# Optimization experiments

Measured on AMD Instinct MI355X. Metric: run time of the kernel, lower is better.

The kernel has to match this reference:

```python
import jax, jax.numpy as jnp
import numpy as np

N, E, D, H, C = 50000, 1600000, 256, 8, 32

def setup_inputs() -> dict:
    key = jax.random.key(0)
    ks = jax.random.split(key, 7)
    feat = jax.random.normal(ks[0], (N, D), dtype=jnp.float32)
    edge_weight = jax.random.uniform(ks[1], (E,), dtype=jnp.float32)
    W_lin = jax.random.normal(ks[2], (D, H * C), dtype=jnp.float32) * (1.0 / np.sqrt(D))
    att_l = jax.random.normal(ks[3], (1, H, C), dtype=jnp.float32) * (1.0 / np.sqrt(H))
    att_r = jax.random.normal(ks[4], (1, H, C), dtype=jnp.float32) * (1.0 / np.sqrt(H))
    W_res = jax.random.normal(ks[5], (D, H * C), dtype=jnp.float32) * (1.0 / np.sqrt(D))
    edge_index = jax.random.randint(ks[6], (2, E), 0, N, dtype=jnp.int32)
    return {"feat": feat, "edge_weight": edge_weight, "W_lin": W_lin,
            "att_l": att_l, "att_r": att_r, "W_res": W_res, "edge_index": edge_index}

def reference(feat, edge_weight, W_lin, att_l, att_r, W_res, edge_index):
    n_nodes = feat.shape[0]
    h, c = att_l.shape[1], att_l.shape[2]
    src, dst = edge_index[0], edge_index[1]
    # node projection: [N, H, C]
    x = (feat @ W_lin).reshape(n_nodes, h, c)
    alpha_l = (x * att_l).sum(-1)  # [N, H]
    alpha_r = (x * att_r).sum(-1)  # [N, H]
    # per-edge scores [E, H]
    alpha = alpha_l[src] + alpha_r[dst]
    alpha = edge_weight[:, None] * alpha
    alpha = jnp.where(alpha > 0, alpha, 0.2 * alpha)  # leaky_relu(0.2)
    # segment softmax over destination nodes
    amax = jax.lax.stop_gradient(jax.ops.segment_max(alpha, dst, num_segments=n_nodes))
    ex = jnp.exp(alpha - amax[dst])
    denom = jax.ops.segment_sum(ex, dst, num_segments=n_nodes)
    coeff = ex / (denom[dst] + 1e-16)  # [E, H]
    # weighted message aggregation
    msg = x[src] * coeff[:, :, None]  # [E, H, C]
    agg = jax.ops.segment_sum(msg, dst, num_segments=n_nodes)  # [N, H, C]
    out = jax.nn.elu(agg).reshape(n_nodes, h * c)
    out = out + feat @ W_res  # residual
    return out
```

## Files before the change

### kernel.cpp

```cpp
#include <hip/hip_runtime.h>
#include <stdint.h>

#define D_DIM 256
#define NPAD  640

typedef __bf16 bf16x8 __attribute__((ext_vector_type(8)));
typedef float  f32x4  __attribute__((ext_vector_type(4)));

__device__ __forceinline__ float bf2f(unsigned short u) {
  union { unsigned int i; float f; } cv; cv.i = ((unsigned int)u) << 16; return cv.f;
}
__device__ __forceinline__ unsigned short f2bf(float f) {
  union { float f; unsigned int i; } cv; cv.f = f;
  unsigned int i = cv.i;
  unsigned int lsb = (i >> 16) & 1u;
  i += 0x7fffu + lsb;
  return (unsigned short)(i >> 16);
}
__device__ __forceinline__ void gld16(const void* gptr, void* lptr) {
  __builtin_amdgcn_global_load_lds(
      (const __attribute__((address_space(1))) unsigned int*)gptr,
      (__attribute__((address_space(3))) unsigned int*)lptr, 16, 0, 0);
}

__global__ __launch_bounds__(256) void cvt_feat(const float* __restrict__ f,
                                                unsigned short* __restrict__ o, int n) {
  int i = (blockIdx.x * 256 + threadIdx.x) * 8;
  if (i >= n) return;
  float4 v0 = *(const float4*)(f + i);
  float4 v1 = *(const float4*)(f + i + 4);
  ushort4 a, b;
  a.x = f2bf(v0.x); a.y = f2bf(v0.y); a.z = f2bf(v0.z); a.w = f2bf(v0.w);
  b.x = f2bf(v1.x); b.y = f2bf(v1.y); b.z = f2bf(v1.z); b.w = f2bf(v1.w);
  *(ushort4*)(o + i) = a;
  *(ushort4*)(o + i + 4) = b;
}

__global__ __launch_bounds__(256) void prep_bt(
    const float* __restrict__ W_lin, const float* __restrict__ W_res,
    const float* __restrict__ att_l, const float* __restrict__ att_r,
    unsigned short* __restrict__ Bt) {
  int idx = blockIdx.x * 256 + threadIdx.x;
  if (idx >= NPAD * D_DIM) return;
  int n = idx >> 8, k = idx & 255;
  float v = 0.f;
  if (n < 256) v = W_lin[k * 256 + n];
  else if (n < 512) v = W_res[k * 256 + (n - 256)];
  else if (n < 520) {
    int h = n - 512; float s = 0.f;
    #pragma unroll
    for (int c = 0; c < 32; ++c) s += W_lin[k * 256 + h * 32 + c] * att_l[h * 32 + c];
    v = s;
  } else if (n < 528) {
    int h = n - 520; float s = 0.f;
    #pragma unroll
    for (int c = 0; c < 32; ++c) s += W_lin[k * 256 + h * 32 + c] * att_r[h * 32 + c];
    v = s;
  }
  Bt[idx] = f2bf(v);
}

__global__ __launch_bounds__(256) void gemm_mfma(
    const unsigned short* __restrict__ A,
    const unsigned short* __restrict__ Bt,
    float* __restrict__ out, unsigned short* __restrict__ xbf,
    float* __restrict__ alpha_l, float* __restrict__ alpha_r, int M) {
  __shared__ unsigned short As[128 * 32];
  __shared__ unsigned short Bs[128 * 32];
  int tid  = threadIdx.x;
  int w    = tid >> 6, lane = tid & 63;
  int bm   = blockIdx.x * 128, bn = blockIdx.y * 128;
  int wm   = (w & 1) * 64, wn = (w >> 1) * 64;
  int l16  = lane & 15, quad = lane >> 4;

  f32x4 acc[4][4] = {};

  int srow = w * 32 + (lane >> 2);
  int koff = (lane & 3) * 8;

  for (int k0 = 0; k0 < 256; k0 += 32) {
    #pragma unroll
    for (int i = 0; i < 2; ++i) {
      int r  = srow + i * 16;
      int rg = bm + r; if (rg > M - 1) rg = M - 1;
      gld16(A  + (size_t)rg * 256 + k0 + koff, &As[(w * 32 + i * 16) * 32]);
      gld16(Bt + (size_t)(bn + r) * 256 + k0 + koff, &Bs[(w * 32 + i * 16) * 32]);
    }
    __syncthreads();
    bf16x8 a[4], b[4];
    #pragma unroll
    for (int mi = 0; mi < 4; ++mi)
      a[mi] = *(const bf16x8*)&As[(wm + mi * 16 + l16) * 32 + quad * 8];
    #pragma unroll
    for (int ni = 0; ni < 4; ++ni)
      b[ni] = *(const bf16x8*)&Bs[(wn + ni * 16 + l16) * 32 + quad * 8];
    #pragma unroll
    for (int mi = 0; mi < 4; ++mi)
      #pragma unroll
      for (int ni = 0; ni < 4; ++ni)
        acc[mi][ni] = __builtin_amdgcn_mfma_f32_16x16x32_bf16(a[mi], b[ni], acc[mi][ni], 0, 0, 0);
    __syncthreads();
  }

  #pragma unroll
  for (int mi = 0; mi < 4; ++mi) {
    #pragma unroll
    for (int r = 0; r < 4; ++r) {
      int row = bm + wm + mi * 16 + quad * 4 + r;
      if (row >= M) continue;
      #pragma unroll
      for (int ni = 0; ni < 4; ++ni) {
        int n = bn + wn + ni * 16 + l16;
        float v = acc[mi][ni][r];
        if (n < 256)      xbf[(size_t)row * 256 + n] = f2bf(v);
        else if (n < 512) out[(size_t)row * 256 + (n - 256)] = v;
        else if (n < 520) alpha_l[row * 8 + (n - 512)] = v;
        else if (n < 528) alpha_r[row * 8 + (n - 520)] = v;
      }
    }
  }
}

__global__ __launch_bounds__(256) void hist_kernel(const int* __restrict__ dst,
                                                   int* __restrict__ cnt,
                                                   int* __restrict__ rank, int E) {
  int e = blockIdx.x * 256 + threadIdx.x;
  if (e < E) rank[e] = atomicAdd(&cnt[dst[e]], 1);
}

__global__ __launch_bounds__(256) void scan_partial(const int* __restrict__ cnt,
                                                    int* __restrict__ bsum, int N) {
  __shared__ int s[256];
  int t = threadIdx.x;
  int i = blockIdx.x * 256 + t;
  s[t] = (i < N) ? cnt[i] : 0;
  __syncthreads();
  for (int off = 128; off > 0; off >>= 1) {
    if (t < off) s[t] += s[t + off];
    __syncthreads();
  }
  if (t == 0) bsum[blockIdx.x] = s[0];
}

__global__ __launch_bounds__(256) void scan_top(int* __restrict__ bsum, int nb) {
  __shared__ int s[256];
  int t = threadIdx.x;
  int v = (t < nb) ? bsum[t] : 0;
  s[t] = v;
  __syncthreads();
  for (int off = 1; off < 256; off <<= 1) {
    int u = (t >= off) ? s[t - off] : 0;
    __syncthreads();
    s[t] += u;
    __syncthreads();
  }
  if (t < nb) bsum[t] = s[t] - v;
}

__global__ __launch_bounds__(256) void scan_apply(const int* __restrict__ cnt,
                                                  const int* __restrict__ bsum,
                                                  int* __restrict__ row_ptr, int N) {
  __shared__ int s[256];
  int t = threadIdx.x;
  int i = blockIdx.x * 256 + t;
  int v = (i < N) ? cnt[i] : 0;
  s[t] = v;
  __syncthreads();
  for (int off = 1; off < 256; off <<= 1) {
    int u = (t >= off) ? s[t - off] : 0;
    __syncthreads();
    s[t] += u;
    __syncthreads();
  }
  int excl = bsum[blockIdx.x] + s[t] - v;
  if (i < N) {
    row_ptr[i] = excl;
    if (i == N - 1) row_ptr[N] = excl + v;
  }
}

__global__ __launch_bounds__(256) void scatter_kernel(
    const int* __restrict__ eidx, const float* __restrict__ ew,
    const int* __restrict__ row_ptr, const int* __restrict__ rank,
    int2* __restrict__ pairs, int E) {
  int e = blockIdx.x * 256 + threadIdx.x;
  if (e < E) {
    int d = eidx[E + e];
    int pos = row_ptr[d] + rank[e];
    int2 p; p.x = eidx[e]; p.y = __float_as_int(ew[e]);
    pairs[pos] = p;
  }
}

__global__ __launch_bounds__(256) void agg_kernel(
    const int* __restrict__ row_ptr, const int2* __restrict__ pairs,
    const float* __restrict__ alpha_l, const float* __restrict__ alpha_r,
    const unsigned short* __restrict__ xbf, float* __restrict__ out, int N) {
  int node = blockIdx.x * 4 + (threadIdx.x >> 6);
  if (node >= N) return;
  int lane = threadIdx.x & 63;
  int h  = lane >> 3;
  int cb = lane << 2;

  int beg = row_ptr[node], end = row_ptr[node + 1];
  float arv = alpha_r[node * 8 + h];
  float l = 0.f;
  float ac0 = 0.f, ac1 = 0.f, ac2 = 0.f, ac3 = 0.f;
  int last = end - 1;

  for (int jg = beg; jg < end; jg += 4) {
    int idx[4];
    #pragma unroll
    for (int u = 0; u < 4; ++u) {
      int t = jg + u; idx[u] = (t < last) ? t : last;
    }
    int2 q[4];
    #pragma unroll
    for (int u = 0; u < 4; ++u) q[u] = pairs[idx[u]];
    float al[4];
    #pragma unroll
    for (int u = 0; u < 4; ++u) al[u] = alpha_l[(size_t)q[u].x * 8 + h];
    ushort4 xv[4];
    #pragma unroll
    for (int u = 0; u < 4; ++u)
      xv[u] = *(const ushort4*)(xbf + ((size_t)q[u].x << 8) + cb);
    #pragma unroll
    for (int u = 0; u < 4; ++u) {
      float a = __int_as_float(q[u].y) * (al[u] + arv);
      a = (a > 0.f) ? a : 0.2f * a;
      float p = __expf(a);
      p = (jg + u < end) ? p : 0.f;
      l += p;
      ac0 = fmaf(p, bf2f(xv[u].x), ac0);
      ac1 = fmaf(p, bf2f(xv[u].y), ac1);
      ac2 = fmaf(p, bf2f(xv[u].z), ac2);
      ac3 = fmaf(p, bf2f(xv[u].w), ac3);
    }
  }
  float r = 1.0f / (l + 1e-16f);
  float o0 = ac0 * r, o1 = ac1 * r, o2 = ac2 * r, o3 = ac3 * r;
  o0 = (o0 > 0.f) ? o0 : expm1f(o0);
  o1 = (o1 > 0.f) ? o1 : expm1f(o1);
  o2 = (o2 > 0.f) ? o2 : expm1f(o2);
  o3 = (o3 > 0.f) ? o3 : expm1f(o3);
  float4* op = (float4*)(out + ((size_t)node << 8) + cb);
  float4 res = *op;
  res.x += o0; res.y += o1; res.z += o2; res.w += o3;
  *op = res;
}

extern "C" void kernel_launch(void* const* d_in, const int* in_sizes, int n_in,
                              void* d_out, int out_size, void* d_ws, size_t ws_size,
                              hipStream_t stream) {
  const float* feat  = (const float*)d_in[0];
  const float* ew    = (const float*)d_in[1];
  const float* W_lin = (const float*)d_in[2];
  const float* att_l = (const float*)d_in[3];
  const float* att_r = (const float*)d_in[4];
  const float* W_res = (const float*)d_in[5];
  const int*   eidx  = (const int*)d_in[6];
  float* out = (float*)d_out;

  int N = in_sizes[0] / D_DIM;
  int E = in_sizes[1];

  char* p = (char*)d_ws;
  auto alloc = [&](size_t bytes) {
    char* r = p; p += (bytes + 255) & ~(size_t)255; return r;
  };
  unsigned short* xbf  = (unsigned short*)alloc((size_t)N * 256 * 2);
  unsigned short* fb   = (unsigned short*)alloc((size_t)N * 256 * 2);
  float* alpha_l       = (float*)alloc((size_t)N * 8 * 4);
  float* alpha_r       = (float*)alloc((size_t)N * 8 * 4);
  unsigned short* Bt   = (unsigned short*)alloc((size_t)NPAD * D_DIM * 2);
  int*   row_ptr       = (int*)alloc((size_t)(N + 1) * 4);
  int*   cnt           = (int*)alloc((size_t)N * 4);
  int*   rank          = (int*)alloc((size_t)E * 4);
  int*   bsum          = (int*)alloc(1024);
  int2*  pairs         = (int2*)fb;

  int nb = (N + 255) / 256;

  hipMemsetAsync(cnt, 0, (size_t)N * 4, stream);

  cvt_feat<<<(N * 256 / 8 + 255) / 256, 256, 0, stream>>>(feat, fb, N * 256);
  prep_bt<<<(NPAD * D_DIM + 255) / 256, 256, 0, stream>>>(W_lin, W_res, att_l, att_r, Bt);

  hist_kernel<<<(E + 255) / 256, 256, 0, stream>>>(eidx + E, cnt, rank, E);
  scan_partial<<<nb, 256, 0, stream>>>(cnt, bsum, N);
  scan_top<<<1, 256, 0, stream>>>(bsum, nb);
  scan_apply<<<nb, 256, 0, stream>>>(cnt, bsum, row_ptr, N);

  dim3 ggrid((N + 127) / 128, NPAD / 128);
  gemm_mfma<<<ggrid, 256, 0, stream>>>(fb, Bt, out, xbf, alpha_l, alpha_r, N);

  scatter_kernel<<<(E + 255) / 256, 256, 0, stream>>>(eidx, ew, row_ptr, rank, pairs, E);

  agg_kernel<<<(N + 3) / 4, 256, 0, stream>>>(row_ptr, pairs, alpha_l, alpha_r, xbf, out, N);
}
```

Measured before the change: 425.5 us.

## Fuse setup kernels, co-launch GEMM with edge scatter, unroll aggregation by 8

Merges feature conversion, weight packing and the destination histogram into one launch using block-index ranges. The GEMM and the edge scatter share one launch, with pairs moved to their own workspace buffer so the scatter no longer overwrites the bf16 features the GEMM reads. Aggregation now unrolls 8 edges per iteration for more gathers in flight and skips nodes with no edges. Intent is fewer launches and overlap of independent work; the cost is a larger workspace, a fallback path when it does not fit, and higher register pressure in aggregation.

Result: no change. 419.5 us (-1.4%).

```diff
diff --git a/kernel.cpp b/kernel.cpp
--- a/kernel.cpp
+++ b/kernel.cpp
@@ -23,109 +23,46 @@
       (__attribute__((address_space(3))) unsigned int*)lptr, 16, 0, 0);
 }
 
-__global__ __launch_bounds__(256) void cvt_feat(const float* __restrict__ f,
-                                                unsigned short* __restrict__ o, int n) {
-  int i = (blockIdx.x * 256 + threadIdx.x) * 8;
-  if (i >= n) return;
-  float4 v0 = *(const float4*)(f + i);
-  float4 v1 = *(const float4*)(f + i + 4);
-  ushort4 a, b;
-  a.x = f2bf(v0.x); a.y = f2bf(v0.y); a.z = f2bf(v0.z); a.w = f2bf(v0.w);
-  b.x = f2bf(v1.x); b.y = f2bf(v1.y); b.z = f2bf(v1.z); b.w = f2bf(v1.w);
-  *(ushort4*)(o + i) = a;
-  *(ushort4*)(o + i + 4) = b;
-}
-
-__global__ __launch_bounds__(256) void prep_bt(
+__global__ __launch_bounds__(256) void setup_fused(
+    const float* __restrict__ feat, unsigned short* __restrict__ fb,
     const float* __restrict__ W_lin, const float* __restrict__ W_res,
     const float* __restrict__ att_l, const float* __restrict__ att_r,
-    unsigned short* __restrict__ Bt) {
-  int idx = blockIdx.x * 256 + threadIdx.x;
-  if (idx >= NPAD * D_DIM) return;
-  int n = idx >> 8, k = idx & 255;
-  float v = 0.f;
-  if (n < 256) v = W_lin[k * 256 + n];
-  else if (n < 512) v = W_res[k * 256 + (n - 256)];
-  else if (n < 520) {
-    int h = n - 512; float s = 0.f;
-    #pragma unroll
-    for (int c = 0; c < 32; ++c) s += W_lin[k * 256 + h * 32 + c] * att_l[h * 32 + c];
-    v = s;
-  } else if (n < 528) {
-    int h = n - 520; float s = 0.f;
-    #pragma unroll
-    for (int c = 0; c < 32; ++c) s += W_lin[k * 256 + h * 32 + c] * att_r[h * 32 + c];
-    v = s;
-  }
-  Bt[idx] = f2bf(v);
-}
-
-__global__ __launch_bounds__(256) void gemm_mfma(
-    const unsigned short* __restrict__ A,
-    const unsigned short* __restrict__ Bt,
-    float* __restrict__ out, unsigned short* __restrict__ xbf,
-    float* __restrict__ alpha_l, float* __restrict__ alpha_r, int M) {
-  __shared__ unsigned short As[128 * 32];
-  __shared__ unsigned short Bs[128 * 32];
-  int tid  = threadIdx.x;
-  int w    = tid >> 6, lane = tid & 63;
-  int bm   = blockIdx.x * 128, bn = blockIdx.y * 128;
-  int wm   = (w & 1) * 64, wn = (w >> 1) * 64;
-  int l16  = lane & 15, quad = lane >> 4;
-
-  f32x4 acc[4][4] = {};
-
-  int srow = w * 32 + (lane >> 2);
-  int koff = (lane & 3) * 8;
-
-  for (int k0 = 0; k0 < 256; k0 += 32) {
-    #pragma unroll
-    for (int i = 0; i < 2; ++i) {
-      int r  = srow + i * 16;
-      int rg = bm + r; if (rg > M - 1) rg = M - 1;
-      gld16(A  + (size_t)rg * 256 + k0 + koff, &As[(w * 32 + i * 16) * 32]);
-      gld16(Bt + (size_t)(bn + r) * 256 + k0 + koff, &Bs[(w * 32 + i * 16) * 32]);
-    }
-    __syncthreads();
-    bf16x8 a[4], b[4];
-    #pragma unroll
-    for (int mi = 0; mi < 4; ++mi)
-      a[mi] = *(const bf16x8*)&As[(wm + mi * 16 + l16) * 32 + quad * 8];
-    #pragma unroll
-    for (int ni = 0; ni < 4; ++ni)
-      b[ni] = *(const bf16x8*)&Bs[(wn + ni * 16 + l16) * 32 + quad * 8];
-    #pragma unroll
-    for (int mi = 0; mi < 4; ++mi)
-      #pragma unroll
-      for (int ni = 0; ni < 4; ++ni)
-        acc[mi][ni] = __builtin_amdgcn_mfma_f32_16x16x32_bf16(a[mi], b[ni], acc[mi][ni], 0, 0, 0);
-    __syncthreads();
-  }
-
-  #pragma unroll
-  for (int mi = 0; mi < 4; ++mi) {
-    #pragma unroll
-    for (int r = 0; r < 4; ++r) {
-      int row = bm + wm + mi * 16 + quad * 4 + r;
-      if (row >= M) continue;
-      #pragma unroll
-      for (int ni = 0; ni < 4; ++ni) {
-        int n = bn + wn + ni * 16 + l16;
-        float v = acc[mi][ni][r];
-        if (n < 256)      xbf[(size_t)row * 256 + n] = f2bf(v);
-        else if (n < 512) out[(size_t)row * 256 + (n - 256)] = v;
-        else if (n < 520) alpha_l[row * 8 + (n - 512)] = v;
-        else if (n < 528) alpha_r[row * 8 + (n - 520)] = v;
-      }
-    }
-  }
-}
-
-__global__ __launch_bounds__(256) void hist_kernel(const int* __restrict__ dst,
-                                                   int* __restrict__ cnt,
-                                                   int* __restrict__ rank, int E) {
-  int e = blockIdx.x * 256 + threadIdx.x;
-  if (e < E) rank[e] = atomicAdd(&cnt[dst[e]], 1);
+    unsigned short* __restrict__ Bt,
+    const int* __restrict__ dst, int* __restrict__ cnt, int* __restrict__ rank,
+    int nelem, int E, int nb_cvt, int nb_prep) {
+  int bid = blockIdx.x, t = threadIdx.x;
+  if (bid < nb_cvt) {
+    int i = (bid * 256 + t) * 8;
+    if (i >= nelem) return;
+    float4 v0 = *(const float4*)(feat + i);
+    float4 v1 = *(const float4*)(feat + i + 4);
+    ushort4 a, b;
+    a.x = f2bf(v0.x); a.y = f2bf(v0.y); a.z = f2bf(v0.z); a.w = f2bf(v0.w);
+    b.x = f2bf(v1.x); b.y = f2bf(v1.y); b.z = f2bf(v1.z); b.w = f2bf(v1.w);
+    *(ushort4*)(fb + i) = a;
+    *(ushort4*)(fb + i + 4) = b;
+  } else if (bid < nb_cvt + nb_prep) {
+    int idx = (bid - nb_cvt) * 256 + t;
+    int n = idx >> 8, k = idx & 255;
+    float v = 0.f;
+    if (n < 256) v = W_lin[k * 256 + n];
+    else if (n < 512) v = W_res[k * 256 + (n - 256)];
+    else if (n < 520) {
+      int h = n - 512; float s = 0.f;
+      #pragma unroll
+      for (int c = 0; c < 32; ++c) s += W_lin[k * 256 + h * 32 + c] * att_l[h * 32 + c];
+      v = s;
+    } else if (n < 528) {
+      int h = n - 520; float s = 0.f;
+      #pragma unroll
+      for (int c = 0; c < 32; ++c) s += W_lin[k * 256 + h * 32 + c] * att_r[h * 32 + c];
+      v = s;
+    }
+    Bt[idx] = f2bf(v);
+  } else {
+    int e = (bid - nb_cvt - nb_prep) * 256 + t;
+    if (e < E) rank[e] = atomicAdd(&cnt[dst[e]], 1);
+  }
 }
 
 __global__ __launch_bounds__(256) void scan_partial(const int* __restrict__ cnt,
@@ -179,16 +116,79 @@
   }
 }
 
-__global__ __launch_bounds__(256) void scatter_kernel(
+__global__ __launch_bounds__(256) void gemm_scatter(
+    const unsigned short* __restrict__ A,
+    const unsigned short* __restrict__ Bt,
+    float* __restrict__ out, unsigned short* __restrict__ xbf,
+    float* __restrict__ alpha_l, float* __restrict__ alpha_r, int M,
     const int* __restrict__ eidx, const float* __restrict__ ew,
     const int* __restrict__ row_ptr, const int* __restrict__ rank,
-    int2* __restrict__ pairs, int E) {
-  int e = blockIdx.x * 256 + threadIdx.x;
-  if (e < E) {
-    int d = eidx[E + e];
-    int pos = row_ptr[d] + rank[e];
-    int2 p; p.x = eidx[e]; p.y = __float_as_int(ew[e]);
-    pairs[pos] = p;
+    int2* __restrict__ pairs, int E, int gemm_blocks, int gx) {
+  __shared__ unsigned short As[128 * 32];
+  __shared__ unsigned short Bs[128 * 32];
+
+  if ((int)blockIdx.x >= gemm_blocks) {
+    int e = ((int)blockIdx.x - gemm_blocks) * 256 + threadIdx.x;
+    if (e < E) {
+      int d = eidx[E + e];
+      int pos = row_ptr[d] + rank[e];
+      int2 p; p.x = eidx[e]; p.y = __float_as_int(ew[e]);
+      pairs[pos] = p;
+    }
+    return;
+  }
+
+  int tid  = threadIdx.x;
+  int w    = tid >> 6, lane = tid & 63;
+  int bm   = ((int)blockIdx.x % gx) * 128, bn = ((int)blockIdx.x / gx) * 128;
+  int wm   = (w & 1) * 64, wn = (w >> 1) * 64;
+  int l16  = lane & 15, quad = lane >> 4;
+
+  f32x4 acc[4][4] = {};
+
+  int srow = w * 32 + (lane >> 2);
+  int koff = (lane & 3) * 8;
+
+  for (int k0 = 0; k0 < 256; k0 += 32) {
+    #pragma unroll
+    for (int i = 0; i < 2; ++i) {
+      int r  = srow + i * 16;
+      int rg = bm + r; if (rg > M - 1) rg = M - 1;
+      gld16(A  + (size_t)rg * 256 + k0 + koff, &As[(w * 32 + i * 16) * 32]);
+      gld16(Bt + (size_t)(bn + r) * 256 + k0 + koff, &Bs[(w * 32 + i * 16) * 32]);
+    }
+    __syncthreads();
+    bf16x8 a[4], b[4];
+    #pragma unroll
+    for (int mi = 0; mi < 4; ++mi)
+      a[mi] = *(const bf16x8*)&As[(wm + mi * 16 + l16) * 32 + quad * 8];
+    #pragma unroll
+    for (int ni = 0; ni < 4; ++ni)
+      b[ni] = *(const bf16x8*)&Bs[(wn + ni * 16 + l16) * 32 + quad * 8];
+    #pragma unroll
+    for (int mi = 0; mi < 4; ++mi)
+      #pragma unroll
+      for (int ni = 0; ni < 4; ++ni)
+        acc[mi][ni] = __builtin_amdgcn_mfma_f32_16x16x32_bf16(a[mi], b[ni], acc[mi][ni], 0, 0, 0);
+    __syncthreads();
+  }
+
+  #pragma unroll
+  for (int mi = 0; mi < 4; ++mi) {
+    #pragma unroll
+    for (int r = 0; r < 4; ++r) {
+      int row = bm + wm + mi * 16 + quad * 4 + r;
+      if (row >= M) continue;
+      #pragma unroll
+      for (int ni = 0; ni < 4; ++ni) {
+        int n = bn + wn + ni * 16 + l16;
+        float v = acc[mi][ni][r];
+        if (n < 256)      xbf[(size_t)row * 256 + n] = f2bf(v);
+        else if (n < 512) out[(size_t)row * 256 + (n - 256)] = v;
+        else if (n < 520) alpha_l[row * 8 + (n - 512)] = v;
+        else if (n < 528) alpha_r[row * 8 + (n - 520)] = v;
+      }
+    }
   }
 }
 
@@ -206,35 +206,36 @@
   float arv = alpha_r[node * 8 + h];
   float l = 0.f;
   float ac0 = 0.f, ac1 = 0.f, ac2 = 0.f, ac3 = 0.f;
-  int last = end - 1;
-
-  for (int jg = beg; jg < end; jg += 4) {
-    int idx[4];
-    #pragma unroll
-    for (int u = 0; u < 4; ++u) {
-      int t = jg + u; idx[u] = (t < last) ? t : last;
-    }
-    int2 q[4];
-    #pragma unroll
-    for (int u = 0; u < 4; ++u) q[u] = pairs[idx[u]];
-    float al[4];
-    #pragma unroll
-    for (int u = 0; u < 4; ++u) al[u] = alpha_l[(size_t)q[u].x * 8 + h];
-    ushort4 xv[4];
-    #pragma unroll
-    for (int u = 0; u < 4; ++u)
-      xv[u] = *(const ushort4*)(xbf + ((size_t)q[u].x << 8) + cb);
-    #pragma unroll
-    for (int u = 0; u < 4; ++u) {
-      float a = __int_as_float(q[u].y) * (al[u] + arv);
-      a = (a > 0.f) ? a : 0.2f * a;
-      float p = __expf(a);
-      p = (jg + u < end) ? p : 0.f;
-      l += p;
-      ac0 = fmaf(p, bf2f(xv[u].x), ac0);
-      ac1 = fmaf(p, bf2f(xv[u].y), ac1);
-      ac2 = fmaf(p, bf2f(xv[u].z), ac2);
-      ac3 = fmaf(p, bf2f(xv[u].w), ac3);
+
+  if (beg < end) {
+    int last = end - 1;
+    const unsigned short* xb = xbf + cb;
+    for (int jg = beg; jg < end; jg += 8) {
+      int2 q[8];
+      #pragma unroll
+      for (int u = 0; u < 8; ++u) {
+        int t = jg + u; t = (t < last) ? t : last;
+        q[u] = pairs[t];
+      }
+      float al[8];
+      #pragma unroll
+      for (int u = 0; u < 8; ++u) al[u] = alpha_l[(size_t)q[u].x * 8 + h];
+      ushort4 xv[8];
+      #pragma unroll
+      for (int u = 0; u < 8; ++u)
+        xv[u] = *(const ushort4*)(xb + ((size_t)q[u].x << 8));
+      #pragma unroll
+      for (int u = 0; u < 8; ++u) {
+        float a = __int_as_float(q[u].y) * (al[u] + arv);
+        a = (a > 0.f) ? a : 0.2f * a;
+        float p = __expf(a);
+        p = (jg + u < end) ? p : 0.f;
+        l += p;
+        ac0 = fmaf(p, bf2f(xv[u].x), ac0);
+        ac1 = fmaf(p, bf2f(xv[u].y), ac1);
+        ac2 = fmaf(p, bf2f(xv[u].z), ac2);
+        ac3 = fmaf(p, bf2f(xv[u].w), ac3);
+      }
     }
   }
   float r = 1.0f / (l + 1e-16f);
@@ -277,24 +278,39 @@
   int*   cnt           = (int*)alloc((size_t)N * 4);
   int*   rank          = (int*)alloc((size_t)E * 4);
   int*   bsum          = (int*)alloc(1024);
-  int2*  pairs         = (int2*)fb;
-
-  int nb = (N + 255) / 256;
+  int2*  pairs_sep     = (int2*)alloc((size_t)E * 8);
+  bool fused_ok = ((size_t)((char*)(pairs_sep + E) - (char*)d_ws) <= ws_size);
+  int2* pairs = fused_ok ? pairs_sep : (int2*)fb;
+
+  int nb      = (N + 255) / 256;
+  int nb_cvt  = (N * 256 / 8 + 255) / 256;
+  int nb_prep = NPAD * D_DIM / 256;
+  int nb_hist = (E + 255) / 256;
+  int gx = (N + 127) / 128;
+  int gemm_blocks = gx * (NPAD / 128);
 
   hipMemsetAsync(cnt, 0, (size_t)N * 4, stream);
 
-  cvt_feat<<<(N * 256 / 8 + 255) / 256, 256, 0, stream>>>(feat, fb, N * 256);
-  prep_bt<<<(NPAD * D_DIM + 255) / 256, 256, 0, stream>>>(W_lin, W_res, att_l, att_r, Bt);
-
-  hist_kernel<<<(E + 255) / 256, 256, 0, stream>>>(eidx + E, cnt, rank, E);
+  setup_fused<<<nb_cvt + nb_prep + nb_hist, 256, 0, stream>>>(
+      feat, fb, W_lin, W_res, att_l, att_r, Bt, eidx + E, cnt, rank,
+      N * 256, E, nb_cvt, nb_prep);
+
   scan_partial<<<nb, 256, 0, stream>>>(cnt, bsum, N);
   scan_top<<<1, 256, 0, stream>>>(bsum, nb);
   scan_apply<<<nb, 256, 0, stream>>>(cnt, bsum, row_ptr, N);
 
-  dim3 ggrid((N + 127) / 128, NPAD / 128);
-  gemm_mfma<<<ggrid, 256, 0, stream>>>(fb, Bt, out, xbf, alpha_l, alpha_r, N);
-
-  scatter_kernel<<<(E + 255) / 256, 256, 0, stream>>>(eidx, ew, row_ptr, rank, pairs, E);
+  if (fused_ok) {
+    gemm_scatter<<<gemm_blocks + nb_hist, 256, 0, stream>>>(
+        fb, Bt, out, xbf, alpha_l, alpha_r, N,
+        eidx, ew, row_ptr, rank, pairs, E, gemm_blocks, gx);
+  } else {
+    gemm_scatter<<<gemm_blocks, 256, 0, stream>>>(
+        fb, Bt, out, xbf, alpha_l, alpha_r, N,
+        eidx, ew, row_ptr, rank, pairs, 0 , gemm_blocks, gx);
+    gemm_scatter<<<nb_hist, 256, 0, stream>>>(
+        fb, Bt, out, xbf, alpha_l, alpha_r, N,
+        eidx, ew, row_ptr, rank, pairs, E, 0 , gx);
+  }
 
   agg_kernel<<<(N + 3) / 4, 256, 0, stream>>>(row_ptr, pairs, alpha_l, alpha_r, xbf, out, N);
 }
```

## Fuse feature conversion into GEMM, merge scatter into GEMM launch, single-block scan

Applied to the files above, without the earlier changes.

Drops the separate fp32-to-bf16 feature conversion kernel: the GEMM now reads fp32 features and converts them while staging into LDS. The edge scatter work is placed in extra blocks of the GEMM grid so both run in one launch. The three-kernel prefix scan becomes a single 1024-thread block. The histogram is also changed to handle 8 edges per thread. This removes a full feature round-trip through memory and several launches, at the cost of register-staged A loads in the GEMM and a serial per-thread scan over about 49 elements each.

Result: slower. 487.0 us (+14.5%).

```diff
diff --git a/kernel.cpp b/kernel.cpp
--- a/kernel.cpp
+++ b/kernel.cpp
@@ -21,19 +21,6 @@
   __builtin_amdgcn_global_load_lds(
       (const __attribute__((address_space(1))) unsigned int*)gptr,
       (__attribute__((address_space(3))) unsigned int*)lptr, 16, 0, 0);
-}
-
-__global__ __launch_bounds__(256) void cvt_feat(const float* __restrict__ f,
-                                                unsigned short* __restrict__ o, int n) {
-  int i = (blockIdx.x * 256 + threadIdx.x) * 8;
-  if (i >= n) return;
-  float4 v0 = *(const float4*)(f + i);
-  float4 v1 = *(const float4*)(f + i + 4);
-  ushort4 a, b;
-  a.x = f2bf(v0.x); a.y = f2bf(v0.y); a.z = f2bf(v0.z); a.w = f2bf(v0.w);
-  b.x = f2bf(v1.x); b.y = f2bf(v1.y); b.z = f2bf(v1.z); b.w = f2bf(v1.w);
-  *(ushort4*)(o + i) = a;
-  *(ushort4*)(o + i + 4) = b;
 }
 
 __global__ __launch_bounds__(256) void prep_bt(
@@ -60,31 +47,97 @@
   Bt[idx] = f2bf(v);
 }
 
-__global__ __launch_bounds__(256) void gemm_mfma(
-    const unsigned short* __restrict__ A,
+__global__ __launch_bounds__(256) void hist_kernel(const int* __restrict__ dst,
+                                                   int* __restrict__ cnt,
+                                                   int* __restrict__ rank, int E) {
+  int base = blockIdx.x * 2048 + threadIdx.x;
+  #pragma unroll
+  for (int u = 0; u < 8; ++u) {
+    int e = base + u * 256;
+    if (e < E) rank[e] = atomicAdd(&cnt[dst[e]], 1);
+  }
+}
+
+__global__ __launch_bounds__(1024) void scan_one(const int* __restrict__ cnt,
+                                                 int* __restrict__ row_ptr, int N) {
+  __shared__ int sdata[1024];
+  int t = threadIdx.x;
+  int chunk = (N + 1023) >> 10;
+  int b = t * chunk;
+  int e = min(b + chunk, N);
+  int s = 0;
+  for (int i = b; i < e; ++i) s += cnt[i];
+  sdata[t] = s;
+  __syncthreads();
+  for (int off = 1; off < 1024; off <<= 1) {
+    int v = (t >= off) ? sdata[t - off] : 0;
+    __syncthreads();
+    sdata[t] += v;
+    __syncthreads();
+  }
+  int run = sdata[t] - s;
+  for (int i = b; i < e; ++i) { row_ptr[i] = run; run += cnt[i]; }
+  if (t == 1023) row_ptr[N] = sdata[1023];
+}
+
+__global__ __launch_bounds__(256) void gemm_scatter(
+    const float* __restrict__ A32,
     const unsigned short* __restrict__ Bt,
     float* __restrict__ out, unsigned short* __restrict__ xbf,
-    float* __restrict__ alpha_l, float* __restrict__ alpha_r, int M) {
+    float* __restrict__ alpha_l, float* __restrict__ alpha_r, int M,
+    const int* __restrict__ eidx, const float* __restrict__ ew,
+    const int* __restrict__ row_ptr, const int* __restrict__ rank,
+    int2* __restrict__ pairs, int E, int nb_scat, int gx) {
   __shared__ unsigned short As[128 * 32];
   __shared__ unsigned short Bs[128 * 32];
+
+  if ((int)blockIdx.x < nb_scat) {
+    int base = (int)blockIdx.x * 1024 + threadIdx.x;
+    #pragma unroll
+    for (int u = 0; u < 4; ++u) {
+      int e = base + u * 256;
+      if (e < E) {
+        int d = eidx[E + e];
+        int pos = row_ptr[d] + rank[e];
+        int2 p; p.x = eidx[e]; p.y = __float_as_int(ew[e]);
+        pairs[pos] = p;
+      }
+    }
+    return;
+  }
+
   int tid  = threadIdx.x;
   int w    = tid >> 6, lane = tid & 63;
-  int bm   = blockIdx.x * 128, bn = blockIdx.y * 128;
+  int gb   = (int)blockIdx.x - nb_scat;
+  int bm   = (gb % gx) * 128, bn = (gb / gx) * 128;
   int wm   = (w & 1) * 64, wn = (w >> 1) * 64;
   int l16  = lane & 15, quad = lane >> 4;
 
   f32x4 acc[4][4] = {};
 
-  int srow = w * 32 + (lane >> 2);
-  int koff = (lane & 3) * 8;
+  int brow = w * 32 + (lane >> 2);
+  int bkoff = (lane & 3) * 8;
 
   for (int k0 = 0; k0 < 256; k0 += 32) {
     #pragma unroll
+    for (int ps = 0; ps < 2; ++ps) {
+      int idx = ps * 256 + tid;
+      int r   = idx >> 2;
+      int k8  = (idx & 3) * 8;
+      int rg  = bm + r; if (rg > M - 1) rg = M - 1;
+      const float* ap = A32 + (size_t)rg * 256 + k0 + k8;
+      float4 u0 = *(const float4*)ap;
+      float4 u1 = *(const float4*)(ap + 4);
+      ushort4 c0, c1;
+      c0.x = f2bf(u0.x); c0.y = f2bf(u0.y); c0.z = f2bf(u0.z); c0.w = f2bf(u0.w);
+      c1.x = f2bf(u1.x); c1.y = f2bf(u1.y); c1.z = f2bf(u1.z); c1.w = f2bf(u1.w);
+      *(ushort4*)&As[r * 32 + k8]     = c0;
+      *(ushort4*)&As[r * 32 + k8 + 4] = c1;
+    }
+    #pragma unroll
     for (int i = 0; i < 2; ++i) {
-      int r  = srow + i * 16;
-      int rg = bm + r; if (rg > M - 1) rg = M - 1;
-      gld16(A  + (size_t)rg * 256 + k0 + koff, &As[(w * 32 + i * 16) * 32]);
-      gld16(Bt + (size_t)(bn + r) * 256 + k0 + koff, &Bs[(w * 32 + i * 16) * 32]);
+      int r = brow + i * 16;
+      gld16(Bt + (size_t)(bn + r) * 256 + k0 + bkoff, &Bs[(w * 32 + i * 16) * 32]);
     }
     __syncthreads();
     bf16x8 a[4], b[4];
@@ -118,77 +171,6 @@
         else if (n < 528) alpha_r[row * 8 + (n - 520)] = v;
       }
     }
-  }
-}
-
-__global__ __launch_bounds__(256) void hist_kernel(const int* __restrict__ dst,
-                                                   int* __restrict__ cnt,
-                                                   int* __restrict__ rank, int E) {
-  int e = blockIdx.x * 256 + threadIdx.x;
-  if (e < E) rank[e] = atomicAdd(&cnt[dst[e]], 1);
-}
-
-__global__ __launch_bounds__(256) void scan_partial(const int* __restrict__ cnt,
-                                                    int* __restrict__ bsum, int N) {
-  __shared__ int s[256];
-  int t = threadIdx.x;
-  int i = blockIdx.x * 256 + t;
-  s[t] = (i < N) ? cnt[i] : 0;
-  __syncthreads();
-  for (int off = 128; off > 0; off >>= 1) {
-    if (t < off) s[t] += s[t + off];
-    __syncthreads();
-  }
-  if (t == 0) bsum[blockIdx.x] = s[0];
-}
-
-__global__ __launch_bounds__(256) void scan_top(int* __restrict__ bsum, int nb) {
-  __shared__ int s[256];
-  int t = threadIdx.x;
-  int v = (t < nb) ? bsum[t] : 0;
-  s[t] = v;
-  __syncthreads();
-  for (int off = 1; off < 256; off <<= 1) {
-    int u = (t >= off) ? s[t - off] : 0;
-    __syncthreads();
-    s[t] += u;
-    __syncthreads();
-  }
-  if (t < nb) bsum[t] = s[t] - v;
-}
-
-__global__ __launch_bounds__(256) void scan_apply(const int* __restrict__ cnt,
-                                                  const int* __restrict__ bsum,
-                                                  int* __restrict__ row_ptr, int N) {
-  __shared__ int s[256];
-  int t = threadIdx.x;
-  int i = blockIdx.x * 256 + t;
-  int v = (i < N) ? cnt[i] : 0;
-  s[t] = v;
-  __syncthreads();
-  for (int off = 1; off < 256; off <<= 1) {
-    int u = (t >= off) ? s[t - off] : 0;
-    __syncthreads();
-    s[t] += u;
-    __syncthreads();
-  }
-  int excl = bsum[blockIdx.x] + s[t] - v;
-  if (i < N) {
-    row_ptr[i] = excl;
-    if (i == N - 1) row_ptr[N] = excl + v;
-  }
-}
-
-__global__ __launch_bounds__(256) void scatter_kernel(
-    const int* __restrict__ eidx, const float* __restrict__ ew,
-    const int* __restrict__ row_ptr, const int* __restrict__ rank,
-    int2* __restrict__ pairs, int E) {
-  int e = blockIdx.x * 256 + threadIdx.x;
-  if (e < E) {
-    int d = eidx[E + e];
-    int pos = row_ptr[d] + rank[e];
-    int2 p; p.x = eidx[e]; p.y = __float_as_int(ew[e]);
-    pairs[pos] = p;
   }
 }
 
@@ -206,35 +188,36 @@
   float arv = alpha_r[node * 8 + h];
   float l = 0.f;
   float ac0 = 0.f, ac1 = 0.f, ac2 = 0.f, ac3 = 0.f;
-  int last = end - 1;
-
-  for (int jg = beg; jg < end; jg += 4) {
-    int idx[4];
-    #pragma unroll
-    for (int u = 0; u < 4; ++u) {
-      int t = jg + u; idx[u] = (t < last) ? t : last;
-    }
-    int2 q[4];
-    #pragma unroll
-    for (int u = 0; u < 4; ++u) q[u] = pairs[idx[u]];
-    float al[4];
-    #pragma unroll
-    for (int u = 0; u < 4; ++u) al[u] = alpha_l[(size_t)q[u].x * 8 + h];
-    ushort4 xv[4];
-    #pragma unroll
-    for (int u = 0; u < 4; ++u)
-      xv[u] = *(const ushort4*)(xbf + ((size_t)q[u].x << 8) + cb);
-    #pragma unroll
-    for (int u = 0; u < 4; ++u) {
-      float a = __int_as_float(q[u].y) * (al[u] + arv);
-      a = (a > 0.f) ? a : 0.2f * a;
-      float p = __expf(a);
-      p = (jg + u < end) ? p : 0.f;
-      l += p;
-      ac0 = fmaf(p, bf2f(xv[u].x), ac0);
-      ac1 = fmaf(p, bf2f(xv[u].y), ac1);
-      ac2 = fmaf(p, bf2f(xv[u].z), ac2);
-      ac3 = fmaf(p, bf2f(xv[u].w), ac3);
+
+  if (beg < end) {
+    int last = end - 1;
+    const unsigned short* xb = xbf + cb;
+    for (int jg = beg; jg < end; jg += 4) {
+      int2 q[4];
+      #pragma unroll
+      for (int u = 0; u < 4; ++u) {
+        int t = jg + u; t = (t < last) ? t : last;
+        q[u] = pairs[t];
+      }
+      float al[4];
+      #pragma unroll
+      for (int u = 0; u < 4; ++u) al[u] = alpha_l[(size_t)q[u].x * 8 + h];
+      ushort4 xv[4];
+      #pragma unroll
+      for (int u = 0; u < 4; ++u)
+        xv[u] = *(const ushort4*)(xb + ((size_t)q[u].x << 8));
+      #pragma unroll
+      for (int u = 0; u < 4; ++u) {
+        float a = __int_as_float(q[u].y) * (al[u] + arv);
+        a = (a > 0.f) ? a : 0.2f * a;
+        float p = __expf(a);
+        p = (jg + u < end) ? p : 0.f;
+        l += p;
+        ac0 = fmaf(p, bf2f(xv[u].x), ac0);
+        ac1 = fmaf(p, bf2f(xv[u].y), ac1);
+        ac2 = fmaf(p, bf2f(xv[u].z), ac2);
+        ac3 = fmaf(p, bf2f(xv[u].w), ac3);
+      }
     }
   }
   float r = 1.0f / (l + 1e-16f);
@@ -269,32 +252,31 @@
     char* r = p; p += (bytes + 255) & ~(size_t)255; return r;
   };
   unsigned short* xbf  = (unsigned short*)alloc((size_t)N * 256 * 2);
-  unsigned short* fb   = (unsigned short*)alloc((size_t)N * 256 * 2);
   float* alpha_l       = (float*)alloc((size_t)N * 8 * 4);
   float* alpha_r       = (float*)alloc((size_t)N * 8 * 4);
   unsigned short* Bt   = (unsigned short*)alloc((size_t)NPAD * D_DIM * 2);
   int*   row_ptr       = (int*)alloc((size_t)(N + 1) * 4);
   int*   cnt           = (int*)alloc((size_t)N * 4);
   int*   rank          = (int*)alloc((size_t)E * 4);
-  int*   bsum          = (int*)alloc(1024);
-  int2*  pairs         = (int2*)fb;
-
-  int nb = (N + 255) / 256;
+  int2*  pairs         = (int2*)alloc((size_t)E * 8);
+
+  int nb_prep = NPAD * D_DIM / 256;
+  int nb_hist = (E + 2047) / 2048;
+  int nb_scat = (E + 1023) / 1024;
+  int gx = (N + 127) / 128;
+  int gemm_blocks = gx * (NPAD / 128);
 
   hipMemsetAsync(cnt, 0, (size_t)N * 4, stream);
 
-  cvt_feat<<<(N * 256 / 8 + 255) / 256, 256, 0, stream>>>(feat, fb, N * 256);
-  prep_bt<<<(NPAD * D_DIM + 255) / 256, 256, 0, stream>>>(W_lin, W_res, att_l, att_r, Bt);
-
-  hist_kernel<<<(E + 255) / 256, 256, 0, stream>>>(eidx + E, cnt, rank, E);
-  scan_partial<<<nb, 256, 0, stream>>>(cnt, bsum, N);
-  scan_top<<<1, 256, 0, stream>>>(bsum, nb);
-  scan_apply<<<nb, 256, 0, stream>>>(cnt, bsum, row_ptr, N);
-
-  dim3 ggrid((N + 127) / 128, NPAD / 128);
-  gemm_mfma<<<ggrid, 256, 0, stream>>>(fb, Bt, out, xbf, alpha_l, alpha_r, N);
-
-  scatter_kernel<<<(E + 255) / 256, 256, 0, stream>>>(eidx, ew, row_ptr, rank, pairs, E);
+  prep_bt<<<nb_prep, 256, 0, stream>>>(W_lin, W_res, att_l, att_r, Bt);
+
+  hist_kernel<<<nb_hist, 256, 0, stream>>>(eidx + E, cnt, rank, E);
+
+  scan_one<<<1, 1024, 0, stream>>>(cnt, row_ptr, N);
+
+  gemm_scatter<<<nb_scat + gemm_blocks, 256, 0, stream>>>(
+      feat, Bt, out, xbf, alpha_l, alpha_r, N,
+      eidx, ew, row_ptr, rank, pairs, E, nb_scat, gx);
 
   agg_kernel<<<(N + 3) / 4, 256, 0, stream>>>(row_ptr, pairs, alpha_l, alpha_r, xbf, out, N);
 }
```
